# Kernel tuning notes

Measured on AMD Instinct MI355X. Metric: run time of the kernel, lower is better.

## Reference

```python
import jax, jax.numpy as jnp
import numpy as np

N_NODES = 50000
N_EDGES = 800000
D_IN, D_HID, N_CLS = 128, 128, 64


def setup_inputs() -> dict:
    key = jax.random.key(0)
    ks = jax.random.split(key, 12)
    x = jax.random.normal(ks[0], (N_NODES, D_IN), dtype=jnp.float32)
    src = jax.random.randint(ks[1], (N_EDGES,), 0, N_NODES, dtype=jnp.int32)
    dst = jax.random.randint(ks[2], (N_EDGES,), 0, N_NODES, dtype=jnp.int32)
    def lin(k, din, dout):
        s = 1.0 / np.sqrt(din)
        return jax.random.uniform(k, (din, dout), jnp.float32, -s, s)
    dims = [(D_IN, D_HID), (D_HID, D_HID), (D_HID, N_CLS)]
    inp = {"x": x, "src": src, "dst": dst}
    for i, (di, do) in enumerate(dims):
        inp[f"W_self{i}"] = lin(ks[3 + 3 * i], di, do)
        inp[f"W_neigh{i}"] = lin(ks[4 + 3 * i], di, do)
        inp[f"b{i}"] = jnp.zeros((do,), jnp.float32)
    return inp


def _sage_conv(h, src, dst, W_self, W_neigh, b):
    # mean aggregation over incoming neighbors (irregular gather + segment mean)
    msg = h[src]                                             # [E, d]
    agg = jax.ops.segment_sum(msg, dst, num_segments=N_NODES)  # [N, d]
    deg = jax.ops.segment_sum(jnp.ones((src.shape[0],), h.dtype), dst,
                              num_segments=N_NODES)
    mean = agg / jnp.maximum(deg, 1.0)[:, None]
    # DGL SAGEConv('mean'): fc_self(h_dst) + fc_neigh(h_neigh) + bias
    return h @ W_self + mean @ W_neigh + b


def reference(x, src, dst, W_self0, W_neigh0, b0, W_self1, W_neigh1, b1,
              W_self2, W_neigh2, b2):
    h = x
    h = jax.nn.selu(_sage_conv(h, src, dst, W_self0, W_neigh0, b0))
    h = jax.nn.selu(_sage_conv(h, src, dst, W_self1, W_neigh1, b1))
    h = jax.nn.softmax(_sage_conv(h, src, dst, W_self2, W_neigh2, b2), axis=1)
    return h
```

## Files before the change

### kernel.cpp

```cpp
#include <hip/hip_runtime.h>
#include <hip/hip_bf16.h>

#define N_NODES 50000
#define N_EDGES 800000
#define D 128
#define NP4 50048
#define SCAN1_B 782
#define NT_GEMM 782
#define E_CHUNK 2048
#define FILL_CH 391

typedef __attribute__((ext_vector_type(8))) __bf16 bf16x8;
typedef __attribute__((ext_vector_type(4))) float f32x4;

union U8 {
  bf16x8 v;
  uint4 u;
};

__device__ __forceinline__ unsigned short bf16_rne(float x) {
  unsigned u = __builtin_bit_cast(unsigned, x);
  unsigned r = u + 0x7fffu + ((u >> 16) & 1u);
  return (unsigned short)(r >> 16);
}
__device__ __forceinline__ float bf16_f(unsigned short b) {
  unsigned u = ((unsigned)b) << 16;
  return __builtin_bit_cast(float, u);
}
__device__ __forceinline__ void split2(float x, unsigned short& hi, unsigned short& lo) {
  hi = bf16_rne(x);
  lo = bf16_rne(x - bf16_f(hi));
}

__device__ __forceinline__ float selu_f(float x) {
  const float alpha = 1.6732632423543772f;
  const float scale = 1.0507009873554805f;
  return scale * (x > 0.0f ? x : alpha * expm1f(x));
}

__device__ __forceinline__ void splitF(uint4 r0, uint4 r1, U8& ah, U8& al) {
  unsigned u0 = r0.x, u1 = r0.y, u2 = r0.z, u3 = r0.w;
  unsigned u4 = r1.x, u5 = r1.y, u6 = r1.z, u7 = r1.w;
  ah.u.x = (u0 >> 16) | (u1 & 0xffff0000u);
  ah.u.y = (u2 >> 16) | (u3 & 0xffff0000u);
  ah.u.z = (u4 >> 16) | (u5 & 0xffff0000u);
  ah.u.w = (u6 >> 16) | (u7 & 0xffff0000u);
  unsigned r;
#define LOW(u) __builtin_bit_cast(unsigned, __builtin_bit_cast(float, u) - __builtin_bit_cast(float, u & 0xffff0000u))
  r = LOW(u0); al.u.x = r >> 16;
  r = LOW(u1); al.u.x |= r & 0xffff0000u;
  r = LOW(u2); al.u.y = r >> 16;
  r = LOW(u3); al.u.y |= r & 0xffff0000u;
  r = LOW(u4); al.u.z = r >> 16;
  r = LOW(u5); al.u.z |= r & 0xffff0000u;
  r = LOW(u6); al.u.w = r >> 16;
  r = LOW(u7); al.u.w |= r & 0xffff0000u;
#undef LOW
}

__global__ __launch_bounds__(256) void zero_kernel(int* __restrict__ p, int n) {
  int i = blockIdx.x * 256 + threadIdx.x;
  if (i < n) p[i] = 0;
}

__global__ __launch_bounds__(256) void hist_kernel(const int* __restrict__ dst,
                                                   int* __restrict__ cnt) {
  const int cls = blockIdx.x & 7;
  const int base = (blockIdx.x >> 3) * E_CHUNK + threadIdx.x;
#pragma unroll
  for (int i = 0; i < E_CHUNK / 256; ++i) {
    int e = base + i * 256;
    if (e < N_EDGES) {
      int d = dst[e];
      if (((d >> 4) & 7) == cls) atomicAdd(&cnt[(e & 3) * NP4 + d], 1);
    }
  }
}

__global__ __launch_bounds__(256) void scan1_kernel(const int* __restrict__ cnt,
                                                    int* __restrict__ cur,
                                                    int* __restrict__ bsum) {
  __shared__ int s[256];
  const int t = threadIdx.x;
  const int j = blockIdx.x * 256 + t;
  const int n = j >> 2, p = j & 3;
  int v = (n < N_NODES) ? cnt[p * NP4 + n] : 0;
  s[t] = v;
  __syncthreads();
#pragma unroll
  for (int off = 1; off < 256; off <<= 1) {
    int u = (t >= off) ? s[t - off] : 0;
    __syncthreads();
    s[t] += u;
    __syncthreads();
  }
  if (n < N_NODES) cur[p * NP4 + n] = s[t] - v;
  if (t == 255) bsum[blockIdx.x] = s[255];
}

__global__ __launch_bounds__(1024) void scan2_kernel(int* __restrict__ bsum) {
  __shared__ int s[1024];
  const int t = threadIdx.x;
  int v = (t < SCAN1_B) ? bsum[t] : 0;
  s[t] = v;
  __syncthreads();
  for (int off = 1; off < 1024; off <<= 1) {
    int u = (t >= off) ? s[t - off] : 0;
    __syncthreads();
    s[t] += u;
    __syncthreads();
  }
  if (t < SCAN1_B) bsum[t] = s[t] - v;
}

__global__ __launch_bounds__(256) void scan3_kernel(int* __restrict__ cur,
                                                    int* __restrict__ rowptr,
                                                    const int* __restrict__ bsum) {
  const int j = blockIdx.x * 256 + threadIdx.x;
  const int n = j >> 2, p = j & 3;
  if (n < N_NODES) {
    int v = cur[p * NP4 + n] + bsum[blockIdx.x];
    cur[p * NP4 + n] = v;
    if (p == 0) rowptr[n] = v;
  }
}

__global__ __launch_bounds__(256) void fill_kernel(const int* __restrict__ src,
                                                   const int* __restrict__ dst,
                                                   int* __restrict__ cur,
                                                   int* __restrict__ csr_src) {
  const int cls = blockIdx.x & 7;
  const int base = (blockIdx.x >> 3) * E_CHUNK + threadIdx.x;
#pragma unroll
  for (int i = 0; i < E_CHUNK / 256; ++i) {
    int e = base + i * 256;
    if (e < N_EDGES) {
      int d = dst[e];
      if (((d >> 4) & 7) == cls) {
        int pos = atomicAdd(&cur[(e & 3) * NP4 + d], 1);
        csr_src[pos] = src[e];
      }
    }
  }
}

__global__ __launch_bounds__(256) void wsplit_kernel(
    const float* __restrict__ Ws0, const float* __restrict__ Wn0,
    const float* __restrict__ Ws1, const float* __restrict__ Wn1,
    const float* __restrict__ Ws2, const float* __restrict__ Wn2,
    unsigned short* __restrict__ wb) {
  int idx = blockIdx.x * 256 + threadIdx.x;
  if (idx < 32768) {
    int n = idx >> 7, k = idx & 127;
    float wv = (n < 128) ? Ws0[k * 128 + n] : Wn0[k * 128 + (n - 128)];
    unsigned short h, l; split2(wv, h, l);
    int si = idx ^ ((n & 7) << 3);
    wb[si] = h; wb[32768 + si] = l;
  } else if (idx < 65536) {
    int j = idx - 32768;
    int n = j >> 7, k = j & 127;
    float wv = (n < 128) ? Ws1[k * 128 + n] : Wn1[k * 128 + (n - 128)];
    unsigned short h, l; split2(wv, h, l);
    int si = j ^ ((n & 7) << 3);
    wb[65536 + si] = h; wb[98304 + si] = l;
  } else if (idx < 81920) {
    int j = idx - 65536;
    int n = j >> 7, k = j & 127;
    float wv = (n < 64) ? Ws2[k * 64 + n] : Wn2[k * 64 + (n - 64)];
    unsigned short h, l; split2(wv, h, l);
    int si = j ^ ((n & 7) << 3);
    wb[131072 + si] = h; wb[147456 + si] = l;
  }
}

__global__ __launch_bounds__(256, 2) void gemm_dual2(const float* __restrict__ hsrc,
                                                     const unsigned short* __restrict__ wth,
                                                     const unsigned short* __restrict__ wtl,
                                                     const float* __restrict__ bias,
                                                     float* __restrict__ out0,
                                                     unsigned short* __restrict__ out1) {
  constexpr int K = 128;
  __shared__ unsigned short bh_s[128 * K];
  __shared__ unsigned short bl_s[128 * K];

  const int tid = threadIdx.x;
  const int w = tid >> 6;
  const int l = tid & 63;
  const int lr = l & 15;
  const int lg = l >> 4;
  const int row0 = blockIdx.x * 64;
  const int arow = min(row0 + w * 16 + lr, N_NODES - 1);

  uint4 a[8];
  {
    const uint4* hp = (const uint4*)(hsrc + (size_t)arow * D);
#pragma unroll
    for (int q = 0; q < 2; ++q)
#pragma unroll
      for (int kt = 0; kt < 2; ++kt) {
        a[q * 4 + kt * 2 + 0] = hp[q * 16 + kt * 8 + lg * 2];
        a[q * 4 + kt * 2 + 1] = hp[q * 16 + kt * 8 + lg * 2 + 1];
      }
  }

#pragma unroll
  for (int cb = 0; cb < 2; ++cb) {
    if (cb) __syncthreads();
    {
      const uint4* gh = (const uint4*)(wth + (size_t)cb * 128 * K);
      const uint4* gl = (const uint4*)(wtl + (size_t)cb * 128 * K);
      uint4* sh = (uint4*)bh_s;
      uint4* sl = (uint4*)bl_s;
#pragma unroll
      for (int i = 0; i < 8; ++i) {
        sh[tid + i * 256] = gh[tid + i * 256];
        sl[tid + i * 256] = gl[tid + i * 256];
      }
    }
    __syncthreads();

    f32x4 accA[8], accB[8];
#pragma unroll
    for (int i = 0; i < 8; ++i) {
      accA[i] = (f32x4){0.f, 0.f, 0.f, 0.f};
      accB[i] = (f32x4){0.f, 0.f, 0.f, 0.f};
    }

#pragma unroll
    for (int q = 0; q < 2; ++q) {
#pragma unroll
      for (int kt = 0; kt < 2; ++kt) {
        U8 ah, al;
        splitF(a[q * 4 + kt * 2], a[q * 4 + kt * 2 + 1], ah, al);
        const int kb = q * 64 + (((((kt << 2) | lg)) ^ (lr & 7)) << 3);
#pragma unroll
        for (int nf = 0; nf < 8; ++nf) {
          const int si = (nf * 16 + lr) * K + kb;
          bf16x8 bh = *(const bf16x8*)&bh_s[si];
          bf16x8 bl = *(const bf16x8*)&bl_s[si];
          accA[nf] = __builtin_amdgcn_mfma_f32_16x16x32_bf16(ah.v, bh, accA[nf], 0, 0, 0);
          accB[nf] = __builtin_amdgcn_mfma_f32_16x16x32_bf16(al.v, bh, accB[nf], 0, 0, 0);
          accB[nf] = __builtin_amdgcn_mfma_f32_16x16x32_bf16(ah.v, bl, accB[nf], 0, 0, 0);
        }
      }
    }

#pragma unroll
    for (int nf = 0; nf < 8; ++nf) {
      const int col = nf * 16 + lr;
      const float bv = (cb == 0) ? bias[col] : 0.0f;
#pragma unroll
      for (int i = 0; i < 4; ++i) {
        const int grow = row0 + w * 16 + lg * 4 + i;
        if (grow < N_NODES) {
          float v = accA[nf][i] + accB[nf][i];
          if (cb == 0) {
            out0[(size_t)grow * 128 + col] = v + bv;
          } else {
            out1[(size_t)grow * 128 + col] = bf16_rne(v);
          }
        }
      }
    }
  }
}

template <int TC, int ZC>
__global__ __launch_bounds__(256, 2) void gemm_dual(const float* __restrict__ hsrc,
                                                    const unsigned short* __restrict__ wth,
                                                    const unsigned short* __restrict__ wtl,
                                                    const float* __restrict__ bias,
                                                    float* __restrict__ out0,
                                                    unsigned short* __restrict__ out1) {
  constexpr int K = 128;
  __shared__ unsigned short bh_s[128 * K];
  __shared__ unsigned short bl_s[128 * K];

  const int tid = threadIdx.x;
  const int w = tid >> 6;
  const int l = tid & 63;
  const int lr = l & 15;
  const int lg = l >> 4;
  const int cb = blockIdx.y;
  const int colbase = cb * 128;
  const int row0 = blockIdx.x * 64;
  const int arow = min(row0 + w * 16 + lr, N_NODES - 1);

  uint4 a[8];
  {
    const uint4* hp = (const uint4*)(hsrc + (size_t)arow * D);
#pragma unroll
    for (int q = 0; q < 2; ++q)
#pragma unroll
      for (int kt = 0; kt < 2; ++kt) {
        a[q * 4 + kt * 2 + 0] = hp[q * 16 + kt * 8 + lg * 2];
        a[q * 4 + kt * 2 + 1] = hp[q * 16 + kt * 8 + lg * 2 + 1];
      }
  }

  {
    const uint4* gh = (const uint4*)(wth + (size_t)colbase * K);
    const uint4* gl = (const uint4*)(wtl + (size_t)colbase * K);
    uint4* sh = (uint4*)bh_s;
    uint4* sl = (uint4*)bl_s;
#pragma unroll
    for (int i = 0; i < 8; ++i) {
      sh[tid + i * 256] = gh[tid + i * 256];
      sl[tid + i * 256] = gl[tid + i * 256];
    }
  }
  __syncthreads();

  f32x4 accA[8], accB[8];
#pragma unroll
  for (int i = 0; i < 8; ++i) {
    accA[i] = (f32x4){0.f, 0.f, 0.f, 0.f};
    accB[i] = (f32x4){0.f, 0.f, 0.f, 0.f};
  }

#pragma unroll
  for (int q = 0; q < 2; ++q) {
#pragma unroll
    for (int kt = 0; kt < 2; ++kt) {
      U8 ah, al;
      splitF(a[q * 4 + kt * 2], a[q * 4 + kt * 2 + 1], ah, al);
      const int kb = q * 64 + (((((kt << 2) | lg)) ^ (lr & 7)) << 3);
#pragma unroll
      for (int nf = 0; nf < 8; ++nf) {
        const int si = (nf * 16 + lr) * K + kb;
        bf16x8 bh = *(const bf16x8*)&bh_s[si];
        bf16x8 bl = *(const bf16x8*)&bl_s[si];
        accA[nf] = __builtin_amdgcn_mfma_f32_16x16x32_bf16(ah.v, bh, accA[nf], 0, 0, 0);
        accB[nf] = __builtin_amdgcn_mfma_f32_16x16x32_bf16(al.v, bh, accB[nf], 0, 0, 0);
        accB[nf] = __builtin_amdgcn_mfma_f32_16x16x32_bf16(ah.v, bl, accB[nf], 0, 0, 0);
      }
    }
  }

#pragma unroll
  for (int nf = 0; nf < 8; ++nf) {
    const int col = colbase + nf * 16 + lr;
#pragma unroll
    for (int i = 0; i < 4; ++i) {
      const int grow = row0 + w * 16 + lg * 4 + i;
      if (grow < N_NODES) {
        float v = accA[nf][i] + accB[nf][i];
        if (col < ZC) {
          out0[(size_t)grow * ZC + col] = v + bias[col];
        } else {
          out1[(size_t)grow * (TC - ZC) + (col - ZC)] = bf16_rne(v);
        }
      }
    }
  }
}

__global__ __launch_bounds__(256) void gather_act(const unsigned short* __restrict__ zb,
                                                  const float* __restrict__ selfb,
                                                  const int* __restrict__ rowptr,
                                                  const int* __restrict__ csr,
                                                  float* __restrict__ hnext) {
  const int n = blockIdx.x * 8 + (threadIdx.x >> 5);
  const int sl = threadIdx.x & 31;
  const int start = rowptr[n];
  const int end = (n < N_NODES - 1) ? rowptr[n + 1] : N_EDGES;
  const ushort4* zp = (const ushort4*)zb + sl;
  float ax = 0.f, ay = 0.f, az = 0.f, aw = 0.f;
#define ACC4(v) { ax += bf16_f(v.x); ay += bf16_f(v.y); az += bf16_f(v.z); aw += bf16_f(v.w); }
  int e = start;
  for (; e + 7 < end; e += 8) {
    int s0 = csr[e],     s1 = csr[e + 1], s2 = csr[e + 2], s3 = csr[e + 3];
    int s4 = csr[e + 4], s5 = csr[e + 5], s6 = csr[e + 6], s7 = csr[e + 7];
    ushort4 v0 = zp[(size_t)s0 * 32];
    ushort4 v1 = zp[(size_t)s1 * 32];
    ushort4 v2 = zp[(size_t)s2 * 32];
    ushort4 v3 = zp[(size_t)s3 * 32];
    ushort4 v4 = zp[(size_t)s4 * 32];
    ushort4 v5 = zp[(size_t)s5 * 32];
    ushort4 v6 = zp[(size_t)s6 * 32];
    ushort4 v7 = zp[(size_t)s7 * 32];
    ACC4(v0) ACC4(v1) ACC4(v2) ACC4(v3) ACC4(v4) ACC4(v5) ACC4(v6) ACC4(v7)
  }
  if (e + 3 < end) {
    int s0 = csr[e], s1 = csr[e + 1], s2 = csr[e + 2], s3 = csr[e + 3];
    ushort4 v0 = zp[(size_t)s0 * 32];
    ushort4 v1 = zp[(size_t)s1 * 32];
    ushort4 v2 = zp[(size_t)s2 * 32];
    ushort4 v3 = zp[(size_t)s3 * 32];
    ACC4(v0) ACC4(v1) ACC4(v2) ACC4(v3)
    e += 4;
  }
  for (; e < end; ++e) {
    ushort4 v0 = zp[(size_t)csr[e] * 32];
    ACC4(v0)
  }
#undef ACC4
  float inv = 1.0f / (float)max(end - start, 1);
  float4 sv = *(const float4*)(selfb + (size_t)n * D + sl * 4);
  float4 o;
  o.x = selu_f(sv.x + ax * inv);
  o.y = selu_f(sv.y + ay * inv);
  o.z = selu_f(sv.z + az * inv);
  o.w = selu_f(sv.w + aw * inv);
  *(float4*)(hnext + (size_t)n * D + sl * 4) = o;
}

__global__ __launch_bounds__(256) void gather_sm(const unsigned short* __restrict__ z2,
                                                 const float* __restrict__ u,
                                                 const int* __restrict__ rowptr,
                                                 const int* __restrict__ csr,
                                                 float* __restrict__ out) {
  const int n = blockIdx.x * 8 + (threadIdx.x >> 5);
  const int sl = threadIdx.x & 31;
  const int start = rowptr[n];
  const int end = (n < N_NODES - 1) ? rowptr[n + 1] : N_EDGES;
  const ushort2* zp = (const ushort2*)z2 + sl;
  float ax = 0.f, ay = 0.f;
#define ACC2(v) { ax += bf16_f(v.x); ay += bf16_f(v.y); }
  int e = start;
  for (; e + 7 < end; e += 8) {
    int s0 = csr[e],     s1 = csr[e + 1], s2 = csr[e + 2], s3 = csr[e + 3];
    int s4 = csr[e + 4], s5 = csr[e + 5], s6 = csr[e + 6], s7 = csr[e + 7];
    ushort2 v0 = zp[(size_t)s0 * 32];
    ushort2 v1 = zp[(size_t)s1 * 32];
    ushort2 v2 = zp[(size_t)s2 * 32];
    ushort2 v3 = zp[(size_t)s3 * 32];
    ushort2 v4 = zp[(size_t)s4 * 32];
    ushort2 v5 = zp[(size_t)s5 * 32];
    ushort2 v6 = zp[(size_t)s6 * 32];
    ushort2 v7 = zp[(size_t)s7 * 32];
    ACC2(v0) ACC2(v1) ACC2(v2) ACC2(v3) ACC2(v4) ACC2(v5) ACC2(v6) ACC2(v7)
  }
  if (e + 3 < end) {
    int s0 = csr[e], s1 = csr[e + 1], s2 = csr[e + 2], s3 = csr[e + 3];
    ushort2 v0 = zp[(size_t)s0 * 32];
    ushort2 v1 = zp[(size_t)s1 * 32];
    ushort2 v2 = zp[(size_t)s2 * 32];
    ushort2 v3 = zp[(size_t)s3 * 32];
    ACC2(v0) ACC2(v1) ACC2(v2) ACC2(v3)
    e += 4;
  }
  for (; e < end; ++e) {
    ushort2 v0 = zp[(size_t)csr[e] * 32];
    ACC2(v0)
  }
#undef ACC2
  float inv = 1.0f / (float)max(end - start, 1);
  size_t o = (size_t)n * 64 + sl * 2;
  float vx = u[o] + ax * inv;
  float vy = u[o + 1] + ay * inv;
  float m = fmaxf(vx, vy);
#pragma unroll
  for (int off = 16; off > 0; off >>= 1) m = fmaxf(m, __shfl_xor(m, off, 64));
  float ex = expf(vx - m);
  float ey = expf(vy - m);
  float s = ex + ey;
#pragma unroll
  for (int off = 16; off > 0; off >>= 1) s += __shfl_xor(s, off, 64);
  float r = 1.0f / s;
  out[o] = ex * r;
  out[o + 1] = ey * r;
}

extern "C" void kernel_launch(void* const* d_in, const int* in_sizes, int n_in,
                              void* d_out, int out_size, void* d_ws, size_t ws_size,
                              hipStream_t stream) {
  const float* x   = (const float*)d_in[0];
  const int* src   = (const int*)d_in[1];
  const int* dst   = (const int*)d_in[2];
  const float* Ws0 = (const float*)d_in[3];
  const float* Wn0 = (const float*)d_in[4];
  const float* b0  = (const float*)d_in[5];
  const float* Ws1 = (const float*)d_in[6];
  const float* Wn1 = (const float*)d_in[7];
  const float* b1  = (const float*)d_in[8];
  const float* Ws2 = (const float*)d_in[9];
  const float* Wn2 = (const float*)d_in[10];
  const float* b2  = (const float*)d_in[11];
  float* out = (float*)d_out;

  char* ws = (char*)d_ws;
  int* rowptr = (int*)ws;
  int* csr    = (int*)(ws + 200192);
  float* h1   = (float*)(ws + 3400192);
  float* h2   = (float*)(ws + 29000192);
  char* Creg  = ws + 54600192;
  float* selfb = (float*)Creg;
  unsigned short* z2 = (unsigned short*)(Creg + 12800000);
  int* cnt     = (int*)Creg;
  int* cursorP = (int*)(Creg + 800768);
  int* bsum    = (int*)(Creg + 1601536);

  unsigned short* zb = (unsigned short*)d_out;

  unsigned short* wb = (unsigned short*)h2;
  unsigned short* wt0h = wb;
  unsigned short* wt0l = wb + 32768;
  unsigned short* wt1h = wb + 65536;
  unsigned short* wt1l = wb + 98304;
  unsigned short* wt2h = wb + 131072;
  unsigned short* wt2l = wb + 147456;

  unsigned short* wt2hc = (unsigned short*)h1;
  unsigned short* wt2lc = wt2hc + 16384;

  zero_kernel<<<SCAN1_B, 256, 0, stream>>>(cnt, 4 * NP4);
  hist_kernel<<<8 * FILL_CH, 256, 0, stream>>>(dst, cnt);
  scan1_kernel<<<SCAN1_B, 256, 0, stream>>>(cnt, cursorP, bsum);
  scan2_kernel<<<1, 1024, 0, stream>>>(bsum);
  scan3_kernel<<<SCAN1_B, 256, 0, stream>>>(cursorP, rowptr, bsum);
  fill_kernel<<<8 * FILL_CH, 256, 0, stream>>>(src, dst, cursorP, csr);
  wsplit_kernel<<<320, 256, 0, stream>>>(Ws0, Wn0, Ws1, Wn1, Ws2, Wn2, wb);

  gemm_dual2<<<NT_GEMM, 256, 0, stream>>>(x, wt0h, wt0l, b0, selfb, zb);
  gather_act<<<6250, 256, 0, stream>>>(zb, selfb, rowptr, csr, h1);

  gemm_dual2<<<NT_GEMM, 256, 0, stream>>>(h1, wt1h, wt1l, b1, selfb, zb);
  hipMemcpyAsync(wt2hc, wt2h, 65536, hipMemcpyDeviceToDevice, stream);
  gather_act<<<6250, 256, 0, stream>>>(zb, selfb, rowptr, csr, h2);

  gemm_dual<128, 64><<<dim3(NT_GEMM, 1), 256, 0, stream>>>(h2, wt2hc, wt2lc, b2, selfb, z2);
  gather_sm<<<6250, 256, 0, stream>>>(z2, selfb, rowptr, csr, out);
}
```

Baseline: 251.2 us.

## Widen gather loads to 16B per lane, use 8 atomic banks, fuse scan passes

```diff
diff --git a/kernel.cpp b/kernel.cpp
--- a/kernel.cpp
+++ b/kernel.cpp
@@ -4,8 +4,9 @@
 #define N_NODES 50000
 #define N_EDGES 800000
 #define D 128
-#define NP4 50048
-#define SCAN1_B 782
+#define NPB 50048
+#define NBANK 8
+#define SCAN1_B 1564
 #define NT_GEMM 782
 #define E_CHUNK 2048
 #define FILL_CH 391
@@ -26,6 +27,12 @@
 __device__ __forceinline__ float bf16_f(unsigned short b) {
   unsigned u = ((unsigned)b) << 16;
   return __builtin_bit_cast(float, u);
+}
+__device__ __forceinline__ float bflo(unsigned u) {
+  return __builtin_bit_cast(float, u << 16);
+}
+__device__ __forceinline__ float bfhi(unsigned u) {
+  return __builtin_bit_cast(float, u & 0xffff0000u);
 }
 __device__ __forceinline__ void split2(float x, unsigned short& hi, unsigned short& lo) {
   hi = bf16_rne(x);
@@ -72,7 +79,7 @@
     int e = base + i * 256;
     if (e < N_EDGES) {
       int d = dst[e];
-      if (((d >> 4) & 7) == cls) atomicAdd(&cnt[(e & 3) * NP4 + d], 1);
+      if (((d >> 4) & 7) == cls) atomicAdd(&cnt[(e & (NBANK - 1)) * NPB + d], 1);
     }
   }
 }
@@ -83,8 +90,8 @@
   __shared__ int s[256];
   const int t = threadIdx.x;
   const int j = blockIdx.x * 256 + t;
-  const int n = j >> 2, p = j & 3;
-  int v = (n < N_NODES) ? cnt[p * NP4 + n] : 0;
+  const int n = j >> 3, p = j & 7;
+  int v = (n < N_NODES) ? cnt[p * NPB + n] : 0;
   s[t] = v;
   __syncthreads();
 #pragma unroll
@@ -94,33 +101,30 @@
     s[t] += u;
     __syncthreads();
   }
-  if (n < N_NODES) cur[p * NP4 + n] = s[t] - v;
+  if (n < N_NODES) cur[p * NPB + n] = s[t] - v;
   if (t == 255) bsum[blockIdx.x] = s[255];
-}
-
-__global__ __launch_bounds__(1024) void scan2_kernel(int* __restrict__ bsum) {
-  __shared__ int s[1024];
-  const int t = threadIdx.x;
-  int v = (t < SCAN1_B) ? bsum[t] : 0;
-  s[t] = v;
-  __syncthreads();
-  for (int off = 1; off < 1024; off <<= 1) {
-    int u = (t >= off) ? s[t - off] : 0;
-    __syncthreads();
-    s[t] += u;
-    __syncthreads();
-  }
-  if (t < SCAN1_B) bsum[t] = s[t] - v;
 }
 
 __global__ __launch_bounds__(256) void scan3_kernel(int* __restrict__ cur,
                                                     int* __restrict__ rowptr,
                                                     const int* __restrict__ bsum) {
-  const int j = blockIdx.x * 256 + threadIdx.x;
-  const int n = j >> 2, p = j & 3;
+  __shared__ int s[256];
+  const int t = threadIdx.x;
+  int part = 0;
+  for (int j = t; j < blockIdx.x; j += 256) part += bsum[j];
+  s[t] = part;
+  __syncthreads();
+#pragma unroll
+  for (int off = 128; off > 0; off >>= 1) {
+    if (t < off) s[t] += s[t + off];
+    __syncthreads();
+  }
+  const int prefix = s[0];
+  const int j = blockIdx.x * 256 + t;
+  const int n = j >> 3, p = j & 7;
   if (n < N_NODES) {
-    int v = cur[p * NP4 + n] + bsum[blockIdx.x];
-    cur[p * NP4 + n] = v;
+    int v = cur[p * NPB + n] + prefix;
+    cur[p * NPB + n] = v;
     if (p == 0) rowptr[n] = v;
   }
 }
@@ -137,7 +141,7 @@
     if (e < N_EDGES) {
       int d = dst[e];
       if (((d >> 4) & 7) == cls) {
-        int pos = atomicAdd(&cur[(e & 3) * NP4 + d], 1);
+        int pos = atomicAdd(&cur[(e & (NBANK - 1)) * NPB + d], 1);
         csr_src[pos] = src[e];
       }
     }
@@ -360,49 +364,59 @@
                                                   const int* __restrict__ rowptr,
                                                   const int* __restrict__ csr,
                                                   float* __restrict__ hnext) {
-  const int n = blockIdx.x * 8 + (threadIdx.x >> 5);
-  const int sl = threadIdx.x & 31;
+  const int n = blockIdx.x * 16 + (threadIdx.x >> 4);
+  const int sl = threadIdx.x & 15;
   const int start = rowptr[n];
   const int end = (n < N_NODES - 1) ? rowptr[n + 1] : N_EDGES;
-  const ushort4* zp = (const ushort4*)zb + sl;
-  float ax = 0.f, ay = 0.f, az = 0.f, aw = 0.f;
-#define ACC4(v) { ax += bf16_f(v.x); ay += bf16_f(v.y); az += bf16_f(v.z); aw += bf16_f(v.w); }
+  const uint4* zp = (const uint4*)zb + sl;
+  float a0 = 0.f, a1 = 0.f, a2 = 0.f, a3 = 0.f;
+  float a4 = 0.f, a5 = 0.f, a6 = 0.f, a7 = 0.f;
+#define ACCU(v) { a0 += bflo(v.x); a1 += bfhi(v.x); a2 += bflo(v.y); a3 += bfhi(v.y); \
+                  a4 += bflo(v.z); a5 += bfhi(v.z); a6 += bflo(v.w); a7 += bfhi(v.w); }
   int e = start;
   for (; e + 7 < end; e += 8) {
     int s0 = csr[e],     s1 = csr[e + 1], s2 = csr[e + 2], s3 = csr[e + 3];
     int s4 = csr[e + 4], s5 = csr[e + 5], s6 = csr[e + 6], s7 = csr[e + 7];
-    ushort4 v0 = zp[(size_t)s0 * 32];
-    ushort4 v1 = zp[(size_t)s1 * 32];
-    ushort4 v2 = zp[(size_t)s2 * 32];
-    ushort4 v3 = zp[(size_t)s3 * 32];
-    ushort4 v4 = zp[(size_t)s4 * 32];
-    ushort4 v5 = zp[(size_t)s5 * 32];
-    ushort4 v6 = zp[(size_t)s6 * 32];
-    ushort4 v7 = zp[(size_t)s7 * 32];
-    ACC4(v0) ACC4(v1) ACC4(v2) ACC4(v3) ACC4(v4) ACC4(v5) ACC4(v6) ACC4(v7)
+    uint4 v0 = zp[(size_t)s0 * 16];
+    uint4 v1 = zp[(size_t)s1 * 16];
+    uint4 v2 = zp[(size_t)s2 * 16];
+    uint4 v3 = zp[(size_t)s3 * 16];
+    uint4 v4 = zp[(size_t)s4 * 16];
+    uint4 v5 = zp[(size_t)s5 * 16];
+    uint4 v6 = zp[(size_t)s6 * 16];
+    uint4 v7 = zp[(size_t)s7 * 16];
+    ACCU(v0) ACCU(v1) ACCU(v2) ACCU(v3) ACCU(v4) ACCU(v5) ACCU(v6) ACCU(v7)
   }
   if (e + 3 < end) {
     int s0 = csr[e], s1 = csr[e + 1], s2 = csr[e + 2], s3 = csr[e + 3];
-    ushort4 v0 = zp[(size_t)s0 * 32];
-    ushort4 v1 = zp[(size_t)s1 * 32];
-    ushort4 v2 = zp[(size_t)s2 * 32];
-    ushort4 v3 = zp[(size_t)s3 * 32];
-    ACC4(v0) ACC4(v1) ACC4(v2) ACC4(v3)
+    uint4 v0 = zp[(size_t)s0 * 16];
+    uint4 v1 = zp[(size_t)s1 * 16];
+    uint4 v2 = zp[(size_t)s2 * 16];
+    uint4 v3 = zp[(size_t)s3 * 16];
+    ACCU(v0) ACCU(v1) ACCU(v2) ACCU(v3)
     e += 4;
   }
   for (; e < end; ++e) {
-    ushort4 v0 = zp[(size_t)csr[e] * 32];
-    ACC4(v0)
-  }
-#undef ACC4
+    uint4 v0 = zp[(size_t)csr[e] * 16];
+    ACCU(v0)
+  }
+#undef ACCU
   float inv = 1.0f / (float)max(end - start, 1);
-  float4 sv = *(const float4*)(selfb + (size_t)n * D + sl * 4);
-  float4 o;
-  o.x = selu_f(sv.x + ax * inv);
-  o.y = selu_f(sv.y + ay * inv);
-  o.z = selu_f(sv.z + az * inv);
-  o.w = selu_f(sv.w + aw * inv);
-  *(float4*)(hnext + (size_t)n * D + sl * 4) = o;
+  const float* sp = selfb + (size_t)n * D + sl * 8;
+  float4 sv0 = *(const float4*)sp;
+  float4 sv1 = *(const float4*)(sp + 4);
+  float4 o0, o1;
+  o0.x = selu_f(sv0.x + a0 * inv);
+  o0.y = selu_f(sv0.y + a1 * inv);
+  o0.z = selu_f(sv0.z + a2 * inv);
+  o0.w = selu_f(sv0.w + a3 * inv);
+  o1.x = selu_f(sv1.x + a4 * inv);
+  o1.y = selu_f(sv1.y + a5 * inv);
+  o1.z = selu_f(sv1.z + a6 * inv);
+  o1.w = selu_f(sv1.w + a7 * inv);
+  float* op = hnext + (size_t)n * D + sl * 8;
+  *(float4*)op = o0;
+  *(float4*)(op + 4) = o1;
 }
 
 __global__ __launch_bounds__(256) void gather_sm(const unsigned short* __restrict__ z2,
@@ -410,56 +424,62 @@
                                                  const int* __restrict__ rowptr,
                                                  const int* __restrict__ csr,
                                                  float* __restrict__ out) {
-  const int n = blockIdx.x * 8 + (threadIdx.x >> 5);
-  const int sl = threadIdx.x & 31;
+  const int n = blockIdx.x * 16 + (threadIdx.x >> 4);
+  const int sl = threadIdx.x & 15;
   const int start = rowptr[n];
   const int end = (n < N_NODES - 1) ? rowptr[n + 1] : N_EDGES;
-  const ushort2* zp = (const ushort2*)z2 + sl;
-  float ax = 0.f, ay = 0.f;
-#define ACC2(v) { ax += bf16_f(v.x); ay += bf16_f(v.y); }
+  const uint2* zp = (const uint2*)z2 + sl;
+  float a0 = 0.f, a1 = 0.f, a2 = 0.f, a3 = 0.f;
+#define ACCU(v) { a0 += bflo(v.x); a1 += bfhi(v.x); a2 += bflo(v.y); a3 += bfhi(v.y); }
   int e = start;
   for (; e + 7 < end; e += 8) {
     int s0 = csr[e],     s1 = csr[e + 1], s2 = csr[e + 2], s3 = csr[e + 3];
     int s4 = csr[e + 4], s5 = csr[e + 5], s6 = csr[e + 6], s7 = csr[e + 7];
-    ushort2 v0 = zp[(size_t)s0 * 32];
-    ushort2 v1 = zp[(size_t)s1 * 32];
-    ushort2 v2 = zp[(size_t)s2 * 32];
-    ushort2 v3 = zp[(size_t)s3 * 32];
-    ushort2 v4 = zp[(size_t)s4 * 32];
-    ushort2 v5 = zp[(size_t)s5 * 32];
-    ushort2 v6 = zp[(size_t)s6 * 32];
-    ushort2 v7 = zp[(size_t)s7 * 32];
-    ACC2(v0) ACC2(v1) ACC2(v2) ACC2(v3) ACC2(v4) ACC2(v5) ACC2(v6) ACC2(v7)
+    uint2 v0 = zp[(size_t)s0 * 16];
+    uint2 v1 = zp[(size_t)s1 * 16];
+    uint2 v2 = zp[(size_t)s2 * 16];
+    uint2 v3 = zp[(size_t)s3 * 16];
+    uint2 v4 = zp[(size_t)s4 * 16];
+    uint2 v5 = zp[(size_t)s5 * 16];
+    uint2 v6 = zp[(size_t)s6 * 16];
+    uint2 v7 = zp[(size_t)s7 * 16];
+    ACCU(v0) ACCU(v1) ACCU(v2) ACCU(v3) ACCU(v4) ACCU(v5) ACCU(v6) ACCU(v7)
   }
   if (e + 3 < end) {
     int s0 = csr[e], s1 = csr[e + 1], s2 = csr[e + 2], s3 = csr[e + 3];
-    ushort2 v0 = zp[(size_t)s0 * 32];
-    ushort2 v1 = zp[(size_t)s1 * 32];
-    ushort2 v2 = zp[(size_t)s2 * 32];
-    ushort2 v3 = zp[(size_t)s3 * 32];
-    ACC2(v0) ACC2(v1) ACC2(v2) ACC2(v3)
+    uint2 v0 = zp[(size_t)s0 * 16];
+    uint2 v1 = zp[(size_t)s1 * 16];
+    uint2 v2 = zp[(size_t)s2 * 16];
+    uint2 v3 = zp[(size_t)s3 * 16];
+    ACCU(v0) ACCU(v1) ACCU(v2) ACCU(v3)
     e += 4;
   }
   for (; e < end; ++e) {
-    ushort2 v0 = zp[(size_t)csr[e] * 32];
-    ACC2(v0)
-  }
-#undef ACC2
+    uint2 v0 = zp[(size_t)csr[e] * 16];
+    ACCU(v0)
+  }
+#undef ACCU
   float inv = 1.0f / (float)max(end - start, 1);
-  size_t o = (size_t)n * 64 + sl * 2;
-  float vx = u[o] + ax * inv;
-  float vy = u[o + 1] + ay * inv;
-  float m = fmaxf(vx, vy);
-#pragma unroll
-  for (int off = 16; off > 0; off >>= 1) m = fmaxf(m, __shfl_xor(m, off, 64));
-  float ex = expf(vx - m);
-  float ey = expf(vy - m);
-  float s = ex + ey;
-#pragma unroll
-  for (int off = 16; off > 0; off >>= 1) s += __shfl_xor(s, off, 64);
+  size_t o = (size_t)n * 64 + sl * 4;
+  float4 uv = *(const float4*)(u + o);
+  float v0 = uv.x + a0 * inv;
+  float v1 = uv.y + a1 * inv;
+  float v2 = uv.z + a2 * inv;
+  float v3 = uv.w + a3 * inv;
+  float m = fmaxf(fmaxf(v0, v1), fmaxf(v2, v3));
+#pragma unroll
+  for (int off = 8; off > 0; off >>= 1) m = fmaxf(m, __shfl_xor(m, off, 16));
+  float e0 = expf(v0 - m);
+  float e1 = expf(v1 - m);
+  float e2 = expf(v2 - m);
+  float e3 = expf(v3 - m);
+  float s = (e0 + e1) + (e2 + e3);
+#pragma unroll
+  for (int off = 8; off > 0; off >>= 1) s += __shfl_xor(s, off, 16);
   float r = 1.0f / s;
-  out[o] = ex * r;
-  out[o + 1] = ey * r;
+  float4 ov;
+  ov.x = e0 * r; ov.y = e1 * r; ov.z = e2 * r; ov.w = e3 * r;
+  *(float4*)(out + o) = ov;
 }
 
 extern "C" void kernel_launch(void* const* d_in, const int* in_sizes, int n_in,
@@ -488,8 +508,8 @@
   float* selfb = (float*)Creg;
   unsigned short* z2 = (unsigned short*)(Creg + 12800000);
   int* cnt     = (int*)Creg;
-  int* cursorP = (int*)(Creg + 800768);
-  int* bsum    = (int*)(Creg + 1601536);
+  int* cursorP = (int*)(Creg + 1601536);
+  int* bsum    = (int*)(Creg + 3203072);
 
   unsigned short* zb = (unsigned short*)d_out;
 
@@ -504,21 +524,20 @@
   unsigned short* wt2hc = (unsigned short*)h1;
   unsigned short* wt2lc = wt2hc + 16384;
 
-  zero_kernel<<<SCAN1_B, 256, 0, stream>>>(cnt, 4 * NP4);
+  zero_kernel<<<SCAN1_B, 256, 0, stream>>>(cnt, NBANK * NPB);
   hist_kernel<<<8 * FILL_CH, 256, 0, stream>>>(dst, cnt);
   scan1_kernel<<<SCAN1_B, 256, 0, stream>>>(cnt, cursorP, bsum);
-  scan2_kernel<<<1, 1024, 0, stream>>>(bsum);
   scan3_kernel<<<SCAN1_B, 256, 0, stream>>>(cursorP, rowptr, bsum);
   fill_kernel<<<8 * FILL_CH, 256, 0, stream>>>(src, dst, cursorP, csr);
   wsplit_kernel<<<320, 256, 0, stream>>>(Ws0, Wn0, Ws1, Wn1, Ws2, Wn2, wb);
 
   gemm_dual2<<<NT_GEMM, 256, 0, stream>>>(x, wt0h, wt0l, b0, selfb, zb);
-  gather_act<<<6250, 256, 0, stream>>>(zb, selfb, rowptr, csr, h1);
+  gather_act<<<3125, 256, 0, stream>>>(zb, selfb, rowptr, csr, h1);
 
   gemm_dual2<<<NT_GEMM, 256, 0, stream>>>(h1, wt1h, wt1l, b1, selfb, zb);
   hipMemcpyAsync(wt2hc, wt2h, 65536, hipMemcpyDeviceToDevice, stream);
-  gather_act<<<6250, 256, 0, stream>>>(zb, selfb, rowptr, csr, h2);
+  gather_act<<<3125, 256, 0, stream>>>(zb, selfb, rowptr, csr, h2);
 
   gemm_dual<128, 64><<<dim3(NT_GEMM, 1), 256, 0, stream>>>(h2, wt2hc, wt2lc, b2, selfb, z2);
-  gather_sm<<<6250, 256, 0, stream>>>(z2, selfb, rowptr, csr, out);
-}
+  gather_sm<<<3125, 256, 0, stream>>>(z2, selfb, rowptr, csr, out);
+}
```

Result: no change. 248.6 us (-1.1%).
